# Kernel tuning notes

Measured on AMD Instinct MI355X. Metric: run time of the kernel, lower is better.

Reference implementation:

```python
import jax, jax.numpy as jnp
import numpy as np

EPS = 1e-06
N_HEADS = 8


def setup_inputs() -> dict:
    key = jax.random.key(0)
    ks = jax.random.split(key, 9)
    B, M, T, C = 2, 64, 256, 512
    s = 0.02
    return {
        "x": jax.random.normal(ks[0], (B, M, T, C), dtype=jnp.float32),
        "Wq": jax.random.normal(ks[1], (C, C), dtype=jnp.float32) * s,
        "bq": jnp.zeros((C,), dtype=jnp.float32),
        "Wk": jax.random.normal(ks[2], (C, C), dtype=jnp.float32) * s,
        "bk": jnp.zeros((C,), dtype=jnp.float32),
        "Wv": jax.random.normal(ks[3], (C, C), dtype=jnp.float32) * s,
        "bv": jnp.zeros((C,), dtype=jnp.float32),
        "Wp": jax.random.normal(ks[4], (C, C), dtype=jnp.float32) * s,
        "bp": jnp.zeros((C,), dtype=jnp.float32),
    }


def _proj_heads(x, W, b, N, D):
    # nn.Linear: x @ W.T + b, then view(B,M,T,N,D).transpose(2,3) -> [B,M,N,T,D]
    B, M, T, C = x.shape
    y = jnp.einsum('bmtc,dc->bmtd', x, W) + b
    return y.reshape(B, M, T, N, D).transpose(0, 1, 3, 2, 4)


def reference(x, Wq, bq, Wk, bk, Wv, bv, Wp, bp):
    B, M, T, C = x.shape
    N = N_HEADS
    D = C // N
    q = _proj_heads(x, Wq, bq, N, D)  # [B,M,N,T,D]
    k = _proj_heads(x, Wk, bk, N, D)
    v = _proj_heads(x, Wv, bv, N, D)
    # ELU+1 feature map
    q = jax.nn.elu(q) + 1.0
    k = jax.nn.elu(k) + 1.0
    # KtV = k^T @ v : [B,M,N,D,D]
    KtV = jnp.einsum('bmntd,bmnte->bmnde', k, v)
    # Z = 1 / (q @ sum_t k + eps) : [B,M,N,T]
    ksum = jnp.sum(k, axis=-2)  # [B,M,N,D]
    z = 1.0 / (jnp.einsum('bmntd,bmnd->bmnt', q, ksum) + EPS)
    # Original does Z.expand(...,D) @ KtV; since Z is constant over the D axis,
    # this equals z[t] * sum_d KtV[d, e] -- compute that directly (faithful math).
    KtV_colsum = jnp.sum(KtV, axis=-2)  # [B,M,N,D]
    V = z[..., None] * KtV_colsum[..., None, :]  # [B,M,N,T,D]
    V = V.transpose(0, 1, 3, 2, 4).reshape(B, M, T, N * D)
    out = jnp.einsum('bmtc,dc->bmtd', V, Wp) + bp
    return out
```

## Files before the change

### kernel.cpp

```cpp
#include <hip/hip_runtime.h>
#include <hip/hip_bf16.h>

#define BM_ 128
#define T_  256
#define C_  512
#define NH  8
#define DH  64

typedef __bf16 bf16;
typedef __attribute__((ext_vector_type(8))) __bf16 bf16x8;
typedef __attribute__((ext_vector_type(4))) float f32x4;

__device__ __forceinline__ float elu1(float v){ return v > 0.f ? v + 1.f : __expf(v); }

__device__ __forceinline__ unsigned short f2bf(float f){
  unsigned u = __float_as_uint(f);
  u += 0x7fffu + ((u >> 16) & 1u);
  return (unsigned short)(u >> 16);
}

__device__ __forceinline__ float bf2f(unsigned short b){
  return __uint_as_float(((unsigned)b) << 16);
}

#define GLOAD16(gptr, lptr) __builtin_amdgcn_global_load_lds( \
  (const __attribute__((address_space(1))) void*)(gptr), \
  (__attribute__((address_space(3))) void*)(lptr), 16, 0, 0)

#define FENCE() asm volatile("" ::: "memory")

__global__ __launch_bounds__(256) void cvt3_kernel(
    const float* __restrict__ a, int na4,
    const float* __restrict__ b, int nb4,
    const float* __restrict__ c, int nc4,
    unsigned short* __restrict__ oa, unsigned short* __restrict__ ob,
    unsigned short* __restrict__ oc)
{
  int i = blockIdx.x * blockDim.x + threadIdx.x;
  int stride = gridDim.x * blockDim.x;
  int total = na4 + nb4 + nc4;
  for (; i < total; i += stride) {
    const float* src; unsigned short* dst; int idx;
    if (i < na4)            { src = a; dst = oa; idx = i; }
    else if (i < na4 + nb4) { src = b; dst = ob; idx = i - na4; }
    else                    { src = c; dst = oc; idx = i - na4 - nb4; }
    float4 v = reinterpret_cast<const float4*>(src)[idx];
    ushort4 o;
    o.x = f2bf(v.x); o.y = f2bf(v.y); o.z = f2bf(v.z); o.w = f2bf(v.w);
    reinterpret_cast<ushort4*>(dst)[idx] = o;
  }
}

template<int MODE>
__global__ __launch_bounds__(512, 2) void gemm_proj(
    const bf16* __restrict__ A, const bf16* __restrict__ Bw,
    const float* __restrict__ bias,
    float* __restrict__ krow, float* __restrict__ ksum2,
    const float* __restrict__ ksum2_in, float* __restrict__ zden)
{
  __shared__ bf16 As[2][256 * 64];
  __shared__ bf16 Bs[2][256 * 64];

  const int tid  = threadIdx.x;
  const int lane = tid & 63;
  const int wid  = tid >> 6;
  const int wr   = wid >> 2, wc = wid & 3;

  const int L  = ((blockIdx.x & 7) << 5) + (blockIdx.x >> 3);
  const int tn = L & 1, tm = L >> 1;

  const bf16* Ab = A  + (size_t)(tm * 256) * C_;
  const bf16* Bb = Bw + (size_t)(tn * 256) * C_;

  const int srow  = tid >> 3;
  const int sslot = tid & 7;
  const int fr = lane & 15, fq = lane >> 4;

  f32x4 acc[8][4];
#pragma unroll
  for (int m = 0; m < 8; ++m)
#pragma unroll
    for (int n = 0; n < 4; ++n) acc[m][n] = (f32x4){0.f, 0.f, 0.f, 0.f};

#define STG(XS, Xb, b, h, kt) do { \
  _Pragma("unroll") \
  for (int q = 0; q < 2; ++q) { \
    int r_ = (h) * 128 + q * 64 + srow; \
    GLOAD16(Xb + (size_t)r_ * C_ + (kt) * 64 + ((sslot ^ (r_ & 7)) << 3), \
            &XS[b][(((h) * 128 + q * 64) << 6) + (tid << 3)]); \
  } } while (0)

#define LOFF(row, sl) (((row) << 6) + ((((sl) ^ ((row) & 7))) << 3))

  STG(As, Ab, 0, 0, 0); STG(As, Ab, 0, 1, 0);
  STG(Bs, Bb, 0, 0, 0); STG(Bs, Bb, 0, 1, 0);
  asm volatile("s_waitcnt vmcnt(0)" ::: "memory");
  __builtin_amdgcn_s_barrier();
  FENCE();

  bf16x8 af[4][2], bfr[4][2];

  for (int t = 0; t < 8; ++t) {
    const int cur = t & 1;
    const bool pre = (t < 7);
#pragma unroll
    for (int m = 0; m < 4; ++m)
#pragma unroll
      for (int kk = 0; kk < 2; ++kk) {
        int row = wr * 128 + m * 16 + fr;
        af[m][kk] = *reinterpret_cast<const bf16x8*>(&As[cur][LOFF(row, kk * 4 + fq)]);
      }
#pragma unroll
    for (int n = 0; n < 2; ++n)
#pragma unroll
      for (int kk = 0; kk < 2; ++kk) {
        int row = wc * 64 + n * 16 + fr;
        bfr[n][kk] = *reinterpret_cast<const bf16x8*>(&Bs[cur][LOFF(row, kk * 4 + fq)]);
      }
    if (pre) { STG(As, Ab, cur ^ 1, 0, t + 1); STG(Bs, Bb, cur ^ 1, 0, t + 1); }
    __builtin_amdgcn_s_setprio(1);
#pragma unroll
    for (int m = 0; m < 4; ++m)
#pragma unroll
      for (int n = 0; n < 2; ++n)
#pragma unroll
        for (int kk = 0; kk < 2; ++kk)
          acc[m][n] = __builtin_amdgcn_mfma_f32_16x16x32_bf16(af[m][kk], bfr[n][kk], acc[m][n], 0, 0, 0);
    __builtin_amdgcn_s_setprio(0);
    __builtin_amdgcn_s_barrier();
    FENCE();
#pragma unroll
    for (int n = 0; n < 2; ++n)
#pragma unroll
      for (int kk = 0; kk < 2; ++kk) {
        int row = wc * 64 + (n + 2) * 16 + fr;
        bfr[n + 2][kk] = *reinterpret_cast<const bf16x8*>(&Bs[cur][LOFF(row, kk * 4 + fq)]);
      }
    if (pre) STG(As, Ab, cur ^ 1, 1, t + 1);
    __builtin_amdgcn_s_setprio(1);
#pragma unroll
    for (int m = 0; m < 4; ++m)
#pragma unroll
      for (int n = 0; n < 2; ++n)
#pragma unroll
        for (int kk = 0; kk < 2; ++kk)
          acc[m][n + 2] = __builtin_amdgcn_mfma_f32_16x16x32_bf16(af[m][kk], bfr[n + 2][kk], acc[m][n + 2], 0, 0, 0);
    __builtin_amdgcn_s_setprio(0);
    __builtin_amdgcn_s_barrier();
    FENCE();
#pragma unroll
    for (int m = 0; m < 4; ++m)
#pragma unroll
      for (int kk = 0; kk < 2; ++kk) {
        int row = wr * 128 + 64 + m * 16 + fr;
        af[m][kk] = *reinterpret_cast<const bf16x8*>(&As[cur][LOFF(row, kk * 4 + fq)]);
      }
    if (pre) STG(Bs, Bb, cur ^ 1, 1, t + 1);
    __builtin_amdgcn_s_setprio(1);
#pragma unroll
    for (int m = 0; m < 4; ++m)
#pragma unroll
      for (int n = 0; n < 2; ++n)
#pragma unroll
        for (int kk = 0; kk < 2; ++kk)
          acc[m + 4][n] = __builtin_amdgcn_mfma_f32_16x16x32_bf16(af[m][kk], bfr[n][kk], acc[m + 4][n], 0, 0, 0);
    __builtin_amdgcn_s_setprio(0);
    __builtin_amdgcn_s_barrier();
    FENCE();
    __builtin_amdgcn_s_setprio(1);
#pragma unroll
    for (int m = 0; m < 4; ++m)
#pragma unroll
      for (int n = 0; n < 2; ++n)
#pragma unroll
        for (int kk = 0; kk < 2; ++kk)
          acc[m + 4][n + 2] = __builtin_amdgcn_mfma_f32_16x16x32_bf16(af[m][kk], bfr[n + 2][kk], acc[m + 4][n + 2], 0, 0, 0);
    __builtin_amdgcn_s_setprio(0);
    asm volatile("s_waitcnt vmcnt(0)" ::: "memory");
    __builtin_amdgcn_s_barrier();
    FENCE();
  }
#undef STG
#undef LOFF

  const int bm   = tm;
  const int head = tn * 4 + wc;
  float bj[4];
#pragma unroll
  for (int n = 0; n < 4; ++n) bj[n] = bias[tn * 256 + wc * 64 + n * 16 + fr];

  if (MODE == 0) {
    float cs[4] = {0.f, 0.f, 0.f, 0.f};
#pragma unroll
    for (int m = 0; m < 8; ++m) {
#pragma unroll
      for (int r = 0; r < 4; ++r) {
        float rs = 0.f;
#pragma unroll
        for (int n = 0; n < 4; ++n) {
          float v = elu1(acc[m][n][r] + bj[n]);
          rs += v;
          cs[n] += v;
        }
#pragma unroll
        for (int msk = 1; msk < 16; msk <<= 1) rs += __shfl_xor(rs, msk);
        if (fr == 0) {
          int tg = wr * 128 + m * 16 + fq * 4 + r;
          krow[((size_t)bm * NH + head) * T_ + tg] = rs;
        }
      }
    }
#pragma unroll
    for (int n = 0; n < 4; ++n) {
      cs[n] += __shfl_xor(cs[n], 16);
      cs[n] += __shfl_xor(cs[n], 32);
      if (fq == 0)
        ksum2[((size_t)wr * BM_ + bm) * C_ + tn * 256 + wc * 64 + n * 16 + fr] = cs[n];
    }
  } else {
    float ks[4];
#pragma unroll
    for (int n = 0; n < 4; ++n) {
      size_t col = (size_t)bm * C_ + tn * 256 + wc * 64 + n * 16 + fr;
      ks[n] = ksum2_in[col] + ksum2_in[(size_t)BM_ * C_ + col];
    }
#pragma unroll
    for (int m = 0; m < 8; ++m) {
#pragma unroll
      for (int r = 0; r < 4; ++r) {
        float zs = 0.f;
#pragma unroll
        for (int n = 0; n < 4; ++n) zs = fmaf(elu1(acc[m][n][r] + bj[n]), ks[n], zs);
#pragma unroll
        for (int msk = 1; msk < 16; msk <<= 1) zs += __shfl_xor(zs, msk);
        if (fr == 0) {
          int tg = wr * 128 + m * 16 + fq * 4 + r;
          zden[((size_t)bm * NH + head) * T_ + tg] = zs;
        }
      }
    }
  }
}

__global__ __launch_bounds__(256) void xk_kernel(
    const unsigned short* __restrict__ xb, const float* __restrict__ krow,
    float* __restrict__ xk4, float* __restrict__ srow4)
{
  const int bm = blockIdx.x, qt = blockIdx.y, tid = threadIdx.x;
  __shared__ float krs[NH * 64];
#pragma unroll
  for (int p = 0; p < 2; ++p) {
    int idx = tid + p * 256;
    int n = idx >> 6, t = idx & 63;
    krs[idx] = krow[((size_t)bm * NH + n) * T_ + qt * 64 + t];
  }
  __syncthreads();
  float a0[8], a1[8];
#pragma unroll
  for (int n = 0; n < 8; ++n) { a0[n] = 0.f; a1[n] = 0.f; }
  const unsigned short* xp = xb + ((size_t)bm * T_ + qt * 64) * C_ + tid * 2;
  for (int t = 0; t < 64; ++t) {
    ushort2 u = *reinterpret_cast<const ushort2*>(xp + (size_t)t * C_);
    float x0 = bf2f(u.x), x1 = bf2f(u.y);
#pragma unroll
    for (int n = 0; n < 8; ++n) {
      float kr = krs[n * 64 + t];
      a0[n] = fmaf(kr, x0, a0[n]);
      a1[n] = fmaf(kr, x1, a1[n]);
    }
  }
#pragma unroll
  for (int n = 0; n < 8; ++n)
    *reinterpret_cast<float2*>(&xk4[(((size_t)qt * BM_ + bm) * NH + n) * C_ + tid * 2])
        = make_float2(a0[n], a1[n]);
  if (tid < 8) {
    float s = 0.f;
    for (int t = 0; t < 64; ++t) s += krs[tid * 64 + t];
    srow4[((size_t)qt * BM_ + bm) * NH + tid] = s;
  }
}

__global__ __launch_bounds__(256) void colsum_kernel(
    const float* __restrict__ xk4, const float* __restrict__ srow4,
    const float* __restrict__ Wv, const float* __restrict__ bv,
    float* __restrict__ cs_g)
{
  const int bm0 = blockIdx.x * 8, h = blockIdx.y, tid = threadIdx.x;
  __shared__ float4 xs4[8][128];
#pragma unroll
  for (int p = 0; p < 4; ++p) {
    int idx = tid + p * 256;
    int bmr = idx >> 7, c4 = idx & 127;
    float4 s = make_float4(0.f, 0.f, 0.f, 0.f);
#pragma unroll
    for (int q = 0; q < 4; ++q) {
      float4 u = *reinterpret_cast<const float4*>(
          xk4 + (((size_t)q * BM_ + bm0 + bmr) * NH + h) * C_ + c4 * 4);
      s.x += u.x; s.y += u.y; s.z += u.z; s.w += u.w;
    }
    xs4[bmr][c4] = s;
  }
  __syncthreads();
  const int e = tid & 63, bs = tid >> 6;
  const float4* wv4 = reinterpret_cast<const float4*>(Wv + (size_t)(h * DH + e) * C_);
  float acc0 = 0.f, acc1 = 0.f;
#pragma unroll 4
  for (int c4 = 0; c4 < 128; ++c4) {
    float4 w = wv4[c4];
    float4 a = xs4[bs * 2][c4];
    float4 b = xs4[bs * 2 + 1][c4];
    acc0 += w.x * a.x + w.y * a.y + w.z * a.z + w.w * a.w;
    acc1 += w.x * b.x + w.y * b.y + w.z * b.z + w.w * b.w;
  }
  float bve = bv[h * DH + e];
  int bmA = bm0 + bs * 2, bmB = bmA + 1;
  float sA = 0.f, sB = 0.f;
#pragma unroll
  for (int q = 0; q < 4; ++q) {
    sA += srow4[((size_t)q * BM_ + bmA) * NH + h];
    sB += srow4[((size_t)q * BM_ + bmB) * NH + h];
  }
  cs_g[((size_t)bmA * NH + h) * DH + e] = acc0 + sA * bve;
  cs_g[((size_t)bmB * NH + h) * DH + e] = acc1 + sB * bve;
}

__global__ __launch_bounds__(256) void wbuf_kernel(
    const float* __restrict__ cs_g, const float* __restrict__ Wp,
    float* __restrict__ wbuf)
{
  const int cpt = blockIdx.x, h = blockIdx.y, bm0 = blockIdx.z * 16;
  const int tid = threadIdx.x;
  __shared__ float4 csL4[16][16];
  {
    int bmr = tid >> 4, e4 = tid & 15;
    csL4[bmr][e4] = *reinterpret_cast<const float4*>(
        cs_g + ((size_t)(bm0 + bmr) * NH + h) * DH + e4 * 4);
  }
  __syncthreads();
  const int cp = cpt * 256 + tid;
  float4 wp[16];
  const float4* wpr = reinterpret_cast<const float4*>(Wp + (size_t)cp * C_ + h * DH);
#pragma unroll
  for (int e4 = 0; e4 < 16; ++e4) wp[e4] = wpr[e4];
#pragma unroll
  for (int bmr = 0; bmr < 16; ++bmr) {
    float acc = 0.f;
#pragma unroll
    for (int e4 = 0; e4 < 16; ++e4) {
      float4 c = csL4[bmr][e4];
      acc += wp[e4].x * c.x + wp[e4].y * c.y + wp[e4].z * c.z + wp[e4].w * c.w;
    }
    wbuf[((size_t)(bm0 + bmr) * NH + h) * C_ + cp] = acc;
  }
}

__global__ __launch_bounds__(256) void out_kernel(
    const float* __restrict__ zden, const float* __restrict__ wbuf,
    const float* __restrict__ bp, float* __restrict__ out)
{
  const int bm = blockIdx.x, tt = blockIdx.y, tid = threadIdx.x;
  __shared__ float zs[NH][64];
#pragma unroll
  for (int p = 0; p < 2; ++p) {
    int idx = tid + p * 256;
    int n = idx >> 6, t = idx & 63;
    zs[n][t] = 1.f / (zden[((size_t)bm * NH + n) * T_ + tt * 64 + t] + 1e-6f);
  }
  float2 wv[8];
  const int c2 = tid * 2;
#pragma unroll
  for (int n = 0; n < 8; ++n)
    wv[n] = *reinterpret_cast<const float2*>(wbuf + ((size_t)bm * NH + n) * C_ + c2);
  float2 bpv = *reinterpret_cast<const float2*>(bp + c2);
  __syncthreads();
  float* ob = out + ((size_t)bm * T_ + tt * 64) * C_;
  for (int t = 0; t < 64; ++t) {
    float o0 = bpv.x, o1 = bpv.y;
#pragma unroll
    for (int n = 0; n < 8; ++n) { float z = zs[n][t]; o0 = fmaf(z, wv[n].x, o0); o1 = fmaf(z, wv[n].y, o1); }
    *reinterpret_cast<float2*>(ob + (size_t)t * C_ + c2) = make_float2(o0, o1);
  }
}

extern "C" void kernel_launch(void* const* d_in, const int* in_sizes, int n_in,
                              void* d_out, int out_size, void* d_ws, size_t ws_size,
                              hipStream_t stream)
{
  const float* x  = (const float*)d_in[0];
  const float* Wq = (const float*)d_in[1];
  const float* bq = (const float*)d_in[2];
  const float* Wk = (const float*)d_in[3];
  const float* bk = (const float*)d_in[4];
  const float* Wv = (const float*)d_in[5];
  const float* bv = (const float*)d_in[6];
  const float* Wp = (const float*)d_in[7];
  const float* bp = (const float*)d_in[8];
  float* out = (float*)d_out;

  float* ws    = (float*)d_ws;
  float* zden  = ws;
  float* ksum2 = zden + 262144;
  float* krow  = ksum2 + 131072;
  float* srow4 = krow + 262144;
  float* xk4   = srow4 + 4096;
  float* cs    = xk4 + 2097152;
  float* wbuf  = cs + 65536;
  unsigned short* xb  = (unsigned short*)(wbuf + 524288);
  unsigned short* wkb = xb + 16777216;
  unsigned short* wqb = wkb + 262144;

  cvt3_kernel<<<2048, 256, 0, stream>>>(x, 16777216 / 4, Wk, 262144 / 4, Wq, 262144 / 4,
                                        xb, wkb, wqb);

  gemm_proj<0><<<256, 512, 0, stream>>>((const bf16*)xb, (const bf16*)wkb, bk,
                                        krow, ksum2, nullptr, nullptr);
  xk_kernel<<<dim3(BM_, 4), 256, 0, stream>>>(xb, krow, xk4, srow4);
  colsum_kernel<<<dim3(16, 8), 256, 0, stream>>>(xk4, srow4, Wv, bv, cs);
  wbuf_kernel<<<dim3(2, 8, 8), 256, 0, stream>>>(cs, Wp, wbuf);
  gemm_proj<1><<<256, 512, 0, stream>>>((const bf16*)xb, (const bf16*)wqb, bq,
                                        nullptr, nullptr, ksum2, zden);
  out_kernel<<<dim3(BM_, 4), 256, 0, stream>>>(zden, wbuf, bp, out);
}
```

Before: 115.9 us.

## Fuse x fp32-to-bf16 conversion into K projection GEMM and merge colsum/wbuf kernels

The first projection GEMM now reads fp32 x directly through registers, converts it to bf16, writes it into LDS, and also stores the bf16 copy to global memory (only from tn==0 blocks) for later kernels. This removes the separate full pass that converted x, and that pass's extra launch. The V-projection colsum and the Wp weighting kernels are merged into one kernel that keeps the intermediate column sums in shared memory. The trade-offs are more register pressure and a loss of asynchronous LDS loads for A in the MODE 0 GEMM, and the merged kernel launches only 64 blocks, which reduces parallelism.

```diff
diff --git a/kernel.cpp b/kernel.cpp
--- a/kernel.cpp
+++ b/kernel.cpp
@@ -29,32 +29,25 @@
 
 #define FENCE() asm volatile("" ::: "memory")
 
-__global__ __launch_bounds__(256) void cvt3_kernel(
-    const float* __restrict__ a, int na4,
-    const float* __restrict__ b, int nb4,
-    const float* __restrict__ c, int nc4,
-    unsigned short* __restrict__ oa, unsigned short* __restrict__ ob,
-    unsigned short* __restrict__ oc)
-{
-  int i = blockIdx.x * blockDim.x + threadIdx.x;
-  int stride = gridDim.x * blockDim.x;
-  int total = na4 + nb4 + nc4;
-  for (; i < total; i += stride) {
-    const float* src; unsigned short* dst; int idx;
-    if (i < na4)            { src = a; dst = oa; idx = i; }
-    else if (i < na4 + nb4) { src = b; dst = ob; idx = i - na4; }
-    else                    { src = c; dst = oc; idx = i - na4 - nb4; }
-    float4 v = reinterpret_cast<const float4*>(src)[idx];
-    ushort4 o;
-    o.x = f2bf(v.x); o.y = f2bf(v.y); o.z = f2bf(v.z); o.w = f2bf(v.w);
-    reinterpret_cast<ushort4*>(dst)[idx] = o;
-  }
+__global__ __launch_bounds__(256) void wcvt_kernel(
+    const float* __restrict__ wk, const float* __restrict__ wq,
+    unsigned short* __restrict__ ok, unsigned short* __restrict__ oq)
+{
+  int i = blockIdx.x * 256 + threadIdx.x;
+  float4 v = reinterpret_cast<const float4*>(wk)[i];
+  ushort4 o;
+  o.x = f2bf(v.x); o.y = f2bf(v.y); o.z = f2bf(v.z); o.w = f2bf(v.w);
+  reinterpret_cast<ushort4*>(ok)[i] = o;
+  v = reinterpret_cast<const float4*>(wq)[i];
+  o.x = f2bf(v.x); o.y = f2bf(v.y); o.z = f2bf(v.z); o.w = f2bf(v.w);
+  reinterpret_cast<ushort4*>(oq)[i] = o;
 }
 
 template<int MODE>
 __global__ __launch_bounds__(512, 2) void gemm_proj(
-    const bf16* __restrict__ A, const bf16* __restrict__ Bw,
-    const float* __restrict__ bias,
+    const bf16* __restrict__ A, const float* __restrict__ Axf,
+    unsigned short* __restrict__ xbout,
+    const bf16* __restrict__ Bw, const float* __restrict__ bias,
     float* __restrict__ krow, float* __restrict__ ksum2,
     const float* __restrict__ ksum2_in, float* __restrict__ zden)
 {
@@ -92,9 +85,40 @@
 
 #define LOFF(row, sl) (((row) << 6) + ((((sl) ^ ((row) & 7))) << 3))
 
-  STG(As, Ab, 0, 0, 0); STG(As, Ab, 0, 1, 0);
-  STG(Bs, Bb, 0, 0, 0); STG(Bs, Bb, 0, 1, 0);
-  asm volatile("s_waitcnt vmcnt(0)" ::: "memory");
+#define AISSUE(LO, HI, h, kt) do { \
+  _Pragma("unroll") \
+  for (int q = 0; q < 2; ++q) { \
+    int r_ = (h) * 128 + q * 64 + srow; \
+    const float* gp = Axf + (size_t)(tm * 256 + r_) * C_ + (kt) * 64 + sslot * 8; \
+    LO[q] = *reinterpret_cast<const float4*>(gp); \
+    HI[q] = *reinterpret_cast<const float4*>(gp + 4); \
+  } } while (0)
+
+#define AWRITE(LO, HI, b, h, kt) do { \
+  _Pragma("unroll") \
+  for (int q = 0; q < 2; ++q) { \
+    int r_ = (h) * 128 + q * 64 + srow; \
+    uint4 v; \
+    v.x = (unsigned)f2bf(LO[q].x) | ((unsigned)f2bf(LO[q].y) << 16); \
+    v.y = (unsigned)f2bf(LO[q].z) | ((unsigned)f2bf(LO[q].w) << 16); \
+    v.z = (unsigned)f2bf(HI[q].x) | ((unsigned)f2bf(HI[q].y) << 16); \
+    v.w = (unsigned)f2bf(HI[q].z) | ((unsigned)f2bf(HI[q].w) << 16); \
+    *reinterpret_cast<uint4*>(&As[b][LOFF(r_, sslot)]) = v; \
+    if (tn == 0) \
+      *reinterpret_cast<uint4*>(xbout + (size_t)(tm * 256 + r_) * C_ + (kt) * 64 + sslot * 8) = v; \
+  } } while (0)
+
+  float4 a0l[2], a0h[2], a1l[2], a1h[2];
+
+  if constexpr (MODE == 0) {
+    AISSUE(a0l, a0h, 0, 0); AISSUE(a1l, a1h, 1, 0);
+    STG(Bs, Bb, 0, 0, 0);   STG(Bs, Bb, 0, 1, 0);
+    AWRITE(a0l, a0h, 0, 0, 0); AWRITE(a1l, a1h, 0, 1, 0);
+  } else {
+    STG(As, Ab, 0, 0, 0); STG(As, Ab, 0, 1, 0);
+    STG(Bs, Bb, 0, 0, 0); STG(Bs, Bb, 0, 1, 0);
+  }
+  asm volatile("s_waitcnt vmcnt(0) lgkmcnt(0)" ::: "memory");
   __builtin_amdgcn_s_barrier();
   FENCE();
 
@@ -117,7 +141,11 @@
         int row = wc * 64 + n * 16 + fr;
         bfr[n][kk] = *reinterpret_cast<const bf16x8*>(&Bs[cur][LOFF(row, kk * 4 + fq)]);
       }
-    if (pre) { STG(As, Ab, cur ^ 1, 0, t + 1); STG(Bs, Bb, cur ^ 1, 0, t + 1); }
+    if (pre) {
+      if constexpr (MODE == 0) AISSUE(a0l, a0h, 0, t + 1);
+      else                     STG(As, Ab, cur ^ 1, 0, t + 1);
+      STG(Bs, Bb, cur ^ 1, 0, t + 1);
+    }
     __builtin_amdgcn_s_setprio(1);
 #pragma unroll
     for (int m = 0; m < 4; ++m)
@@ -136,7 +164,11 @@
         int row = wc * 64 + (n + 2) * 16 + fr;
         bfr[n + 2][kk] = *reinterpret_cast<const bf16x8*>(&Bs[cur][LOFF(row, kk * 4 + fq)]);
       }
-    if (pre) STG(As, Ab, cur ^ 1, 1, t + 1);
+    if (pre) {
+      if constexpr (MODE == 0) AISSUE(a1l, a1h, 1, t + 1);
+      else                     STG(As, Ab, cur ^ 1, 1, t + 1);
+      STG(Bs, Bb, cur ^ 1, 1, t + 1);
+    }
     __builtin_amdgcn_s_setprio(1);
 #pragma unroll
     for (int m = 0; m < 4; ++m)
@@ -155,7 +187,7 @@
         int row = wr * 128 + 64 + m * 16 + fr;
         af[m][kk] = *reinterpret_cast<const bf16x8*>(&As[cur][LOFF(row, kk * 4 + fq)]);
       }
-    if (pre) STG(Bs, Bb, cur ^ 1, 1, t + 1);
+    if (pre) { if constexpr (MODE == 0) AWRITE(a0l, a0h, cur ^ 1, 0, t + 1); }
     __builtin_amdgcn_s_setprio(1);
 #pragma unroll
     for (int m = 0; m < 4; ++m)
@@ -167,6 +199,7 @@
     __builtin_amdgcn_s_setprio(0);
     __builtin_amdgcn_s_barrier();
     FENCE();
+    if (pre) { if constexpr (MODE == 0) AWRITE(a1l, a1h, cur ^ 1, 1, t + 1); }
     __builtin_amdgcn_s_setprio(1);
 #pragma unroll
     for (int m = 0; m < 4; ++m)
@@ -176,12 +209,14 @@
         for (int kk = 0; kk < 2; ++kk)
           acc[m + 4][n + 2] = __builtin_amdgcn_mfma_f32_16x16x32_bf16(af[m][kk], bfr[n + 2][kk], acc[m + 4][n + 2], 0, 0, 0);
     __builtin_amdgcn_s_setprio(0);
-    asm volatile("s_waitcnt vmcnt(0)" ::: "memory");
+    asm volatile("s_waitcnt vmcnt(0) lgkmcnt(0)" ::: "memory");
     __builtin_amdgcn_s_barrier();
     FENCE();
   }
 #undef STG
 #undef LOFF
+#undef AISSUE
+#undef AWRITE
 
   const int bm   = tm;
   const int head = tn * 4 + wc;
@@ -280,15 +315,16 @@
   }
 }
 
-__global__ __launch_bounds__(256) void colsum_kernel(
+__global__ __launch_bounds__(256) void vproj_kernel(
     const float* __restrict__ xk4, const float* __restrict__ srow4,
     const float* __restrict__ Wv, const float* __restrict__ bv,
-    float* __restrict__ cs_g)
-{
-  const int bm0 = blockIdx.x * 8, h = blockIdx.y, tid = threadIdx.x;
-  __shared__ float4 xs4[8][128];
-#pragma unroll
-  for (int p = 0; p < 4; ++p) {
+    const float* __restrict__ Wp, float* __restrict__ wbuf)
+{
+  const int bm0 = blockIdx.x * 16, h = blockIdx.y, tid = threadIdx.x;
+  __shared__ float4 xs4[16][128];
+  __shared__ float cs[16][DH];
+#pragma unroll
+  for (int p = 0; p < 8; ++p) {
     int idx = tid + p * 256;
     int bmr = idx >> 7, c4 = idx & 127;
     float4 s = make_float4(0.f, 0.f, 0.f, 0.f);
@@ -301,56 +337,47 @@
     xs4[bmr][c4] = s;
   }
   __syncthreads();
-  const int e = tid & 63, bs = tid >> 6;
-  const float4* wv4 = reinterpret_cast<const float4*>(Wv + (size_t)(h * DH + e) * C_);
-  float acc0 = 0.f, acc1 = 0.f;
+  {
+    const int e = tid & 63, g = tid >> 6;
+    const float4* wv4 = reinterpret_cast<const float4*>(Wv + (size_t)(h * DH + e) * C_);
+    float acc[4] = {0.f, 0.f, 0.f, 0.f};
 #pragma unroll 4
-  for (int c4 = 0; c4 < 128; ++c4) {
-    float4 w = wv4[c4];
-    float4 a = xs4[bs * 2][c4];
-    float4 b = xs4[bs * 2 + 1][c4];
-    acc0 += w.x * a.x + w.y * a.y + w.z * a.z + w.w * a.w;
-    acc1 += w.x * b.x + w.y * b.y + w.z * b.z + w.w * b.w;
-  }
-  float bve = bv[h * DH + e];
-  int bmA = bm0 + bs * 2, bmB = bmA + 1;
-  float sA = 0.f, sB = 0.f;
-#pragma unroll
-  for (int q = 0; q < 4; ++q) {
-    sA += srow4[((size_t)q * BM_ + bmA) * NH + h];
-    sB += srow4[((size_t)q * BM_ + bmB) * NH + h];
-  }
-  cs_g[((size_t)bmA * NH + h) * DH + e] = acc0 + sA * bve;
-  cs_g[((size_t)bmB * NH + h) * DH + e] = acc1 + sB * bve;
-}
-
-__global__ __launch_bounds__(256) void wbuf_kernel(
-    const float* __restrict__ cs_g, const float* __restrict__ Wp,
-    float* __restrict__ wbuf)
-{
-  const int cpt = blockIdx.x, h = blockIdx.y, bm0 = blockIdx.z * 16;
-  const int tid = threadIdx.x;
-  __shared__ float4 csL4[16][16];
-  {
-    int bmr = tid >> 4, e4 = tid & 15;
-    csL4[bmr][e4] = *reinterpret_cast<const float4*>(
-        cs_g + ((size_t)(bm0 + bmr) * NH + h) * DH + e4 * 4);
+    for (int c4 = 0; c4 < 128; ++c4) {
+      float4 w = wv4[c4];
+#pragma unroll
+      for (int i = 0; i < 4; ++i) {
+        float4 a = xs4[g * 4 + i][c4];
+        acc[i] += w.x * a.x + w.y * a.y + w.z * a.z + w.w * a.w;
+      }
+    }
+    float bve = bv[h * DH + e];
+#pragma unroll
+    for (int i = 0; i < 4; ++i) {
+      int bm = bm0 + g * 4 + i;
+      float s = 0.f;
+#pragma unroll
+      for (int q = 0; q < 4; ++q) s += srow4[((size_t)q * BM_ + bm) * NH + h];
+      cs[g * 4 + i][e] = acc[i] + s * bve;
+    }
   }
   __syncthreads();
-  const int cp = cpt * 256 + tid;
-  float4 wp[16];
-  const float4* wpr = reinterpret_cast<const float4*>(Wp + (size_t)cp * C_ + h * DH);
-#pragma unroll
-  for (int e4 = 0; e4 < 16; ++e4) wp[e4] = wpr[e4];
-#pragma unroll
-  for (int bmr = 0; bmr < 16; ++bmr) {
-    float acc = 0.f;
-#pragma unroll
-    for (int e4 = 0; e4 < 16; ++e4) {
-      float4 c = csL4[bmr][e4];
-      acc += wp[e4].x * c.x + wp[e4].y * c.y + wp[e4].z * c.z + wp[e4].w * c.w;
-    }
-    wbuf[((size_t)(bm0 + bmr) * NH + h) * C_ + cp] = acc;
+#pragma unroll
+  for (int cph = 0; cph < 2; ++cph) {
+    int cp = cph * 256 + tid;
+    const float4* wpr = reinterpret_cast<const float4*>(Wp + (size_t)cp * C_ + h * DH);
+    float4 wp[16];
+#pragma unroll
+    for (int e4 = 0; e4 < 16; ++e4) wp[e4] = wpr[e4];
+#pragma unroll
+    for (int bmr = 0; bmr < 16; ++bmr) {
+      const float* ch = cs[bmr];
+      float acc = 0.f;
+#pragma unroll
+      for (int e4 = 0; e4 < 16; ++e4)
+        acc += wp[e4].x * ch[e4 * 4] + wp[e4].y * ch[e4 * 4 + 1]
+             + wp[e4].z * ch[e4 * 4 + 2] + wp[e4].w * ch[e4 * 4 + 3];
+      wbuf[((size_t)(bm0 + bmr) * NH + h) * C_ + cp] = acc;
+    }
   }
 }
 
@@ -403,21 +430,19 @@
   float* krow  = ksum2 + 131072;
   float* srow4 = krow + 262144;
   float* xk4   = srow4 + 4096;
-  float* cs    = xk4 + 2097152;
-  float* wbuf  = cs + 65536;
+  float* wbuf  = xk4 + 2097152;
   unsigned short* xb  = (unsigned short*)(wbuf + 524288);
   unsigned short* wkb = xb + 16777216;
   unsigned short* wqb = wkb + 262144;
 
-  cvt3_kernel<<<2048, 256, 0, stream>>>(x, 16777216 / 4, Wk, 262144 / 4, Wq, 262144 / 4,
-                                        xb, wkb, wqb);
-
-  gemm_proj<0><<<256, 512, 0, stream>>>((const bf16*)xb, (const bf16*)wkb, bk,
+  wcvt_kernel<<<256, 256, 0, stream>>>(Wk, Wq, wkb, wqb);
+
+  gemm_proj<0><<<256, 512, 0, stream>>>(nullptr, x, xb, (const bf16*)wkb, bk,
                                         krow, ksum2, nullptr, nullptr);
   xk_kernel<<<dim3(BM_, 4), 256, 0, stream>>>(xb, krow, xk4, srow4);
-  colsum_kernel<<<dim3(16, 8), 256, 0, stream>>>(xk4, srow4, Wv, bv, cs);
-  wbuf_kernel<<<dim3(2, 8, 8), 256, 0, stream>>>(cs, Wp, wbuf);
-  gemm_proj<1><<<256, 512, 0, stream>>>((const bf16*)xb, (const bf16*)wqb, bq,
-                                        nullptr, nullptr, ksum2, zden);
+  vproj_kernel<<<dim3(8, 8), 256, 0, stream>>>(xk4, srow4, Wv, bv, Wp, wbuf);
+  gemm_proj<1><<<256, 512, 0, stream>>>((const bf16*)xb, nullptr, nullptr,
+                                        (const bf16*)wqb, bq,
+                                        nullptr, ksum2, ksum2, zden);
   out_kernel<<<dim3(BM_, 4), 256, 0, stream>>>(zden, wbuf, bp, out);
 }
```

After: 260.6 us. 125% more time.

## Shrink projection GEMM tiles to 256x128 with K=32 steps for higher occupancy

Applied to the files above, without the earlier changes.

Reworks the bf16 MFMA projection GEMM from 256x256 tiles with K-step 64 to 256x128 tiles with K-step 32. This halves LDS use and accumulators, raises launch bounds to 4 blocks per CU, and doubles the grid to 512 blocks. The key column partial sums are now split into four row-slices instead of two, and the Q pass sums all four. It aims for better CU fill and latency hiding, at the cost of lower per-block data reuse, more global traffic and twice as many barriers per K loop.

```diff
diff --git a/kernel.cpp b/kernel.cpp
--- a/kernel.cpp
+++ b/kernel.cpp
@@ -52,147 +52,94 @@
 }
 
 template<int MODE>
-__global__ __launch_bounds__(512, 2) void gemm_proj(
+__global__ __launch_bounds__(512, 4) void gemm_proj(
     const bf16* __restrict__ A, const bf16* __restrict__ Bw,
     const float* __restrict__ bias,
-    float* __restrict__ krow, float* __restrict__ ksum2,
-    const float* __restrict__ ksum2_in, float* __restrict__ zden)
-{
-  __shared__ bf16 As[2][256 * 64];
-  __shared__ bf16 Bs[2][256 * 64];
+    float* __restrict__ krow, float* __restrict__ ksum4,
+    const float* __restrict__ ksum4_in, float* __restrict__ zden)
+{
+  __shared__ bf16 As[2][256 * 32];
+  __shared__ bf16 Bs[2][128 * 32];
 
   const int tid  = threadIdx.x;
   const int lane = tid & 63;
   const int wid  = tid >> 6;
-  const int wr   = wid >> 2, wc = wid & 3;
-
-  const int L  = ((blockIdx.x & 7) << 5) + (blockIdx.x >> 3);
-  const int tn = L & 1, tm = L >> 1;
+  const int wr   = wid >> 1, wc = wid & 1;
+
+  const int L  = ((blockIdx.x & 7) << 6) + (blockIdx.x >> 3);
+  const int tn = L & 3, tm = L >> 2;
 
   const bf16* Ab = A  + (size_t)(tm * 256) * C_;
-  const bf16* Bb = Bw + (size_t)(tn * 256) * C_;
-
-  const int srow  = tid >> 3;
-  const int sslot = tid & 7;
+  const bf16* Bb = Bw + (size_t)(tn * 128) * C_;
   const int fr = lane & 15, fq = lane >> 4;
 
-  f32x4 acc[8][4];
-#pragma unroll
-  for (int m = 0; m < 8; ++m)
+  f32x4 acc[4][4];
+#pragma unroll
+  for (int m = 0; m < 4; ++m)
 #pragma unroll
     for (int n = 0; n < 4; ++n) acc[m][n] = (f32x4){0.f, 0.f, 0.f, 0.f};
 
-#define STG(XS, Xb, b, h, kt) do { \
+#define SW(r, s) ((s) ^ (((r) ^ ((r) >> 2)) & 3))
+#define LOFF(row, sl) ((row) * 32 + (SW(row, sl) << 3))
+
+#define STGA(b, kt) do { \
   _Pragma("unroll") \
-  for (int q = 0; q < 2; ++q) { \
-    int r_ = (h) * 128 + q * 64 + srow; \
-    GLOAD16(Xb + (size_t)r_ * C_ + (kt) * 64 + ((sslot ^ (r_ & 7)) << 3), \
-            &XS[b][(((h) * 128 + q * 64) << 6) + (tid << 3)]); \
+  for (int j = 0; j < 2; ++j) { \
+    int d_ = j * 512 + tid; int r_ = d_ >> 2; int s_ = d_ & 3; \
+    GLOAD16(Ab + (size_t)r_ * C_ + (kt) * 32 + (SW(r_, s_) << 3), \
+            &As[b][d_ * 8]); \
   } } while (0)
 
-#define LOFF(row, sl) (((row) << 6) + ((((sl) ^ ((row) & 7))) << 3))
-
-  STG(As, Ab, 0, 0, 0); STG(As, Ab, 0, 1, 0);
-  STG(Bs, Bb, 0, 0, 0); STG(Bs, Bb, 0, 1, 0);
+#define STGB(b, kt) do { \
+    int r_ = tid >> 2; int s_ = tid & 3; \
+    GLOAD16(Bb + (size_t)r_ * C_ + (kt) * 32 + (SW(r_, s_) << 3), \
+            &Bs[b][tid * 8]); \
+  } while (0)
+
+  STGA(0, 0); STGB(0, 0);
   asm volatile("s_waitcnt vmcnt(0)" ::: "memory");
   __builtin_amdgcn_s_barrier();
   FENCE();
 
-  bf16x8 af[4][2], bfr[4][2];
-
-  for (int t = 0; t < 8; ++t) {
+  bf16x8 af[4], bfr[4];
+
+  for (int t = 0; t < 16; ++t) {
     const int cur = t & 1;
-    const bool pre = (t < 7);
 #pragma unroll
     for (int m = 0; m < 4; ++m)
-#pragma unroll
-      for (int kk = 0; kk < 2; ++kk) {
-        int row = wr * 128 + m * 16 + fr;
-        af[m][kk] = *reinterpret_cast<const bf16x8*>(&As[cur][LOFF(row, kk * 4 + fq)]);
-      }
-#pragma unroll
-    for (int n = 0; n < 2; ++n)
-#pragma unroll
-      for (int kk = 0; kk < 2; ++kk) {
-        int row = wc * 64 + n * 16 + fr;
-        bfr[n][kk] = *reinterpret_cast<const bf16x8*>(&Bs[cur][LOFF(row, kk * 4 + fq)]);
-      }
-    if (pre) { STG(As, Ab, cur ^ 1, 0, t + 1); STG(Bs, Bb, cur ^ 1, 0, t + 1); }
+      af[m] = *reinterpret_cast<const bf16x8*>(&As[cur][LOFF(wr * 64 + m * 16 + fr, fq)]);
+#pragma unroll
+    for (int n = 0; n < 4; ++n)
+      bfr[n] = *reinterpret_cast<const bf16x8*>(&Bs[cur][LOFF(wc * 64 + n * 16 + fr, fq)]);
+    if (t < 15) { STGA(cur ^ 1, t + 1); STGB(cur ^ 1, t + 1); }
     __builtin_amdgcn_s_setprio(1);
 #pragma unroll
     for (int m = 0; m < 4; ++m)
 #pragma unroll
-      for (int n = 0; n < 2; ++n)
-#pragma unroll
-        for (int kk = 0; kk < 2; ++kk)
-          acc[m][n] = __builtin_amdgcn_mfma_f32_16x16x32_bf16(af[m][kk], bfr[n][kk], acc[m][n], 0, 0, 0);
+      for (int n = 0; n < 4; ++n)
+        acc[m][n] = __builtin_amdgcn_mfma_f32_16x16x32_bf16(af[m], bfr[n], acc[m][n], 0, 0, 0);
     __builtin_amdgcn_s_setprio(0);
-    __builtin_amdgcn_s_barrier();
-    FENCE();
-#pragma unroll
-    for (int n = 0; n < 2; ++n)
-#pragma unroll
-      for (int kk = 0; kk < 2; ++kk) {
-        int row = wc * 64 + (n + 2) * 16 + fr;
-        bfr[n + 2][kk] = *reinterpret_cast<const bf16x8*>(&Bs[cur][LOFF(row, kk * 4 + fq)]);
-      }
-    if (pre) STG(As, Ab, cur ^ 1, 1, t + 1);
-    __builtin_amdgcn_s_setprio(1);
-#pragma unroll
-    for (int m = 0; m < 4; ++m)
-#pragma unroll
-      for (int n = 0; n < 2; ++n)
-#pragma unroll
-        for (int kk = 0; kk < 2; ++kk)
-          acc[m][n + 2] = __builtin_amdgcn_mfma_f32_16x16x32_bf16(af[m][kk], bfr[n + 2][kk], acc[m][n + 2], 0, 0, 0);
-    __builtin_amdgcn_s_setprio(0);
-    __builtin_amdgcn_s_barrier();
-    FENCE();
-#pragma unroll
-    for (int m = 0; m < 4; ++m)
-#pragma unroll
-      for (int kk = 0; kk < 2; ++kk) {
-        int row = wr * 128 + 64 + m * 16 + fr;
-        af[m][kk] = *reinterpret_cast<const bf16x8*>(&As[cur][LOFF(row, kk * 4 + fq)]);
-      }
-    if (pre) STG(Bs, Bb, cur ^ 1, 1, t + 1);
-    __builtin_amdgcn_s_setprio(1);
-#pragma unroll
-    for (int m = 0; m < 4; ++m)
-#pragma unroll
-      for (int n = 0; n < 2; ++n)
-#pragma unroll
-        for (int kk = 0; kk < 2; ++kk)
-          acc[m + 4][n] = __builtin_amdgcn_mfma_f32_16x16x32_bf16(af[m][kk], bfr[n][kk], acc[m + 4][n], 0, 0, 0);
-    __builtin_amdgcn_s_setprio(0);
-    __builtin_amdgcn_s_barrier();
-    FENCE();
-    __builtin_amdgcn_s_setprio(1);
-#pragma unroll
-    for (int m = 0; m < 4; ++m)
-#pragma unroll
-      for (int n = 0; n < 2; ++n)
-#pragma unroll
-        for (int kk = 0; kk < 2; ++kk)
-          acc[m + 4][n + 2] = __builtin_amdgcn_mfma_f32_16x16x32_bf16(af[m][kk], bfr[n + 2][kk], acc[m + 4][n + 2], 0, 0, 0);
-    __builtin_amdgcn_s_setprio(0);
-    asm volatile("s_waitcnt vmcnt(0)" ::: "memory");
-    __builtin_amdgcn_s_barrier();
-    FENCE();
-  }
-#undef STG
+    if (t < 15) {
+      asm volatile("s_waitcnt vmcnt(0)" ::: "memory");
+      __builtin_amdgcn_s_barrier();
+      FENCE();
+    }
+  }
+#undef STGA
+#undef STGB
 #undef LOFF
+#undef SW
 
   const int bm   = tm;
-  const int head = tn * 4 + wc;
+  const int head = tn * 2 + wc;
   float bj[4];
 #pragma unroll
-  for (int n = 0; n < 4; ++n) bj[n] = bias[tn * 256 + wc * 64 + n * 16 + fr];
+  for (int n = 0; n < 4; ++n) bj[n] = bias[tn * 128 + wc * 64 + n * 16 + fr];
 
   if (MODE == 0) {
     float cs[4] = {0.f, 0.f, 0.f, 0.f};
 #pragma unroll
-    for (int m = 0; m < 8; ++m) {
+    for (int m = 0; m < 4; ++m) {
 #pragma unroll
       for (int r = 0; r < 4; ++r) {
         float rs = 0.f;
@@ -205,7 +152,7 @@
 #pragma unroll
         for (int msk = 1; msk < 16; msk <<= 1) rs += __shfl_xor(rs, msk);
         if (fr == 0) {
-          int tg = wr * 128 + m * 16 + fq * 4 + r;
+          int tg = wr * 64 + m * 16 + fq * 4 + r;
           krow[((size_t)bm * NH + head) * T_ + tg] = rs;
         }
       }
@@ -215,17 +162,18 @@
       cs[n] += __shfl_xor(cs[n], 16);
       cs[n] += __shfl_xor(cs[n], 32);
       if (fq == 0)
-        ksum2[((size_t)wr * BM_ + bm) * C_ + tn * 256 + wc * 64 + n * 16 + fr] = cs[n];
+        ksum4[((size_t)wr * BM_ + bm) * C_ + tn * 128 + wc * 64 + n * 16 + fr] = cs[n];
     }
   } else {
     float ks[4];
 #pragma unroll
     for (int n = 0; n < 4; ++n) {
-      size_t col = (size_t)bm * C_ + tn * 256 + wc * 64 + n * 16 + fr;
-      ks[n] = ksum2_in[col] + ksum2_in[(size_t)BM_ * C_ + col];
-    }
-#pragma unroll
-    for (int m = 0; m < 8; ++m) {
+      size_t col = (size_t)bm * C_ + tn * 128 + wc * 64 + n * 16 + fr;
+      ks[n] = ksum4_in[col] + ksum4_in[(size_t)BM_ * C_ + col]
+            + ksum4_in[2 * (size_t)BM_ * C_ + col] + ksum4_in[3 * (size_t)BM_ * C_ + col];
+    }
+#pragma unroll
+    for (int m = 0; m < 4; ++m) {
 #pragma unroll
       for (int r = 0; r < 4; ++r) {
         float zs = 0.f;
@@ -234,7 +182,7 @@
 #pragma unroll
         for (int msk = 1; msk < 16; msk <<= 1) zs += __shfl_xor(zs, msk);
         if (fr == 0) {
-          int tg = wr * 128 + m * 16 + fq * 4 + r;
+          int tg = wr * 64 + m * 16 + fq * 4 + r;
           zden[((size_t)bm * NH + head) * T_ + tg] = zs;
         }
       }
@@ -399,8 +347,8 @@
 
   float* ws    = (float*)d_ws;
   float* zden  = ws;
-  float* ksum2 = zden + 262144;
-  float* krow  = ksum2 + 131072;
+  float* ksum4 = zden + 262144;
+  float* krow  = ksum4 + 262144;
   float* srow4 = krow + 262144;
   float* xk4   = srow4 + 4096;
   float* cs    = xk4 + 2097152;
@@ -412,12 +360,12 @@
   cvt3_kernel<<<2048, 256, 0, stream>>>(x, 16777216 / 4, Wk, 262144 / 4, Wq, 262144 / 4,
                                         xb, wkb, wqb);
 
-  gemm_proj<0><<<256, 512, 0, stream>>>((const bf16*)xb, (const bf16*)wkb, bk,
-                                        krow, ksum2, nullptr, nullptr);
+  gemm_proj<0><<<512, 512, 0, stream>>>((const bf16*)xb, (const bf16*)wkb, bk,
+                                        krow, ksum4, nullptr, nullptr);
   xk_kernel<<<dim3(BM_, 4), 256, 0, stream>>>(xb, krow, xk4, srow4);
   colsum_kernel<<<dim3(16, 8), 256, 0, stream>>>(xk4, srow4, Wv, bv, cs);
   wbuf_kernel<<<dim3(2, 8, 8), 256, 0, stream>>>(cs, Wp, wbuf);
-  gemm_proj<1><<<256, 512, 0, stream>>>((const bf16*)xb, (const bf16*)wqb, bq,
-                                        nullptr, nullptr, ksum2, zden);
+  gemm_proj<1><<<512, 512, 0, stream>>>((const bf16*)xb, (const bf16*)wqb, bq,
+                                        nullptr, ksum4, ksum4, zden);
   out_kernel<<<dim3(BM_, 4), 256, 0, stream>>>(zden, wbuf, bp, out);
 }
```

Measured after the change: 116.6 us. Within noise of the previous version (+0.6%).

## Split GEMM k-tile into half-slices and prefetch two stages ahead

Applied to the files above, without the earlier changes.

Reworks the shared-memory layout of the projection GEMM so each 64-wide k-tile is stored as two 32-wide halves, each with its own XOR swizzle. Loads for the next tile are issued one half at a time, up to two half-stages ahead, and the loop waits with vmcnt(4) instead of fully draining each iteration. Barriers per iteration drop from four to two and fragment registers shrink. The aim is to hide global-load latency behind MFMA work, at the cost of more complex vmcnt bookkeeping and a different bank-conflict pattern. The MODE 1 launch now also passes ksum2 in the ksum2 slot instead of nullptr.

```diff
diff --git a/kernel.cpp b/kernel.cpp
--- a/kernel.cpp
+++ b/kernel.cpp
@@ -58,8 +58,8 @@
     float* __restrict__ krow, float* __restrict__ ksum2,
     const float* __restrict__ ksum2_in, float* __restrict__ zden)
 {
-  __shared__ bf16 As[2][256 * 64];
-  __shared__ bf16 Bs[2][256 * 64];
+  __shared__ bf16 As[2][2 * 8192];
+  __shared__ bf16 Bs[2][2 * 8192];
 
   const int tid  = threadIdx.x;
   const int lane = tid & 63;
@@ -71,9 +71,6 @@
 
   const bf16* Ab = A  + (size_t)(tm * 256) * C_;
   const bf16* Bb = Bw + (size_t)(tn * 256) * C_;
-
-  const int srow  = tid >> 3;
-  const int sslot = tid & 7;
   const int fr = lane & 15, fq = lane >> 4;
 
   f32x4 acc[8][4];
@@ -82,101 +79,83 @@
 #pragma unroll
     for (int n = 0; n < 4; ++n) acc[m][n] = (f32x4){0.f, 0.f, 0.f, 0.f};
 
-#define STG(XS, Xb, b, h, kt) do { \
+#define LOFF(kk, row, sl) ((kk) * 8192 + (row) * 32 + ((((sl) ^ (((row) >> 1) & 3))) << 3))
+
+#define STG(XS, Xb, b, kk, kt) do { \
   _Pragma("unroll") \
-  for (int q = 0; q < 2; ++q) { \
-    int r_ = (h) * 128 + q * 64 + srow; \
-    GLOAD16(Xb + (size_t)r_ * C_ + (kt) * 64 + ((sslot ^ (r_ & 7)) << 3), \
-            &XS[b][(((h) * 128 + q * 64) << 6) + (tid << 3)]); \
+  for (int j = 0; j < 2; ++j) { \
+    int d_ = j * 512 + tid; int r_ = d_ >> 2; int s_ = d_ & 3; \
+    GLOAD16(Xb + (size_t)r_ * C_ + (kt) * 64 + (kk) * 32 + (((s_ ^ ((r_ >> 1) & 3))) << 3), \
+            &XS[b][(kk) * 8192 + d_ * 8]); \
   } } while (0)
 
-#define LOFF(row, sl) (((row) << 6) + ((((sl) ^ ((row) & 7))) << 3))
-
-  STG(As, Ab, 0, 0, 0); STG(As, Ab, 0, 1, 0);
-  STG(Bs, Bb, 0, 0, 0); STG(Bs, Bb, 0, 1, 0);
-  asm volatile("s_waitcnt vmcnt(0)" ::: "memory");
+  STG(As, Ab, 0, 0, 0); STG(Bs, Bb, 0, 0, 0);
+  STG(As, Ab, 0, 1, 0); STG(Bs, Bb, 0, 1, 0);
+  STG(As, Ab, 1, 0, 1); STG(Bs, Bb, 1, 0, 1);
+  asm volatile("s_waitcnt vmcnt(4)" ::: "memory");
   __builtin_amdgcn_s_barrier();
   FENCE();
 
-  bf16x8 af[4][2], bfr[4][2];
+  bf16x8 af[4], bfr[4];
 
   for (int t = 0; t < 8; ++t) {
     const int cur = t & 1;
-    const bool pre = (t < 7);
-#pragma unroll
-    for (int m = 0; m < 4; ++m)
-#pragma unroll
-      for (int kk = 0; kk < 2; ++kk) {
-        int row = wr * 128 + m * 16 + fr;
-        af[m][kk] = *reinterpret_cast<const bf16x8*>(&As[cur][LOFF(row, kk * 4 + fq)]);
-      }
-#pragma unroll
-    for (int n = 0; n < 2; ++n)
-#pragma unroll
-      for (int kk = 0; kk < 2; ++kk) {
-        int row = wc * 64 + n * 16 + fr;
-        bfr[n][kk] = *reinterpret_cast<const bf16x8*>(&Bs[cur][LOFF(row, kk * 4 + fq)]);
-      }
-    if (pre) { STG(As, Ab, cur ^ 1, 0, t + 1); STG(Bs, Bb, cur ^ 1, 0, t + 1); }
+
+#pragma unroll
+    for (int m = 0; m < 4; ++m)
+      af[m] = *reinterpret_cast<const bf16x8*>(&As[cur][LOFF(0, wr * 128 + m * 16 + fr, fq)]);
+#pragma unroll
+    for (int n = 0; n < 4; ++n)
+      bfr[n] = *reinterpret_cast<const bf16x8*>(&Bs[cur][LOFF(0, wc * 64 + n * 16 + fr, fq)]);
+    if (t + 1 < 8) { STG(As, Ab, cur ^ 1, 1, t + 1); STG(Bs, Bb, cur ^ 1, 1, t + 1); }
     __builtin_amdgcn_s_setprio(1);
 #pragma unroll
     for (int m = 0; m < 4; ++m)
 #pragma unroll
-      for (int n = 0; n < 2; ++n)
-#pragma unroll
-        for (int kk = 0; kk < 2; ++kk)
-          acc[m][n] = __builtin_amdgcn_mfma_f32_16x16x32_bf16(af[m][kk], bfr[n][kk], acc[m][n], 0, 0, 0);
+      for (int n = 0; n < 4; ++n)
+        acc[m][n] = __builtin_amdgcn_mfma_f32_16x16x32_bf16(af[m], bfr[n], acc[m][n], 0, 0, 0);
+    __builtin_amdgcn_s_setprio(0);
+
+#pragma unroll
+    for (int m = 0; m < 4; ++m)
+      af[m] = *reinterpret_cast<const bf16x8*>(&As[cur][LOFF(0, wr * 128 + 64 + m * 16 + fr, fq)]);
+    __builtin_amdgcn_s_setprio(1);
+#pragma unroll
+    for (int m = 0; m < 4; ++m)
+#pragma unroll
+      for (int n = 0; n < 4; ++n)
+        acc[m + 4][n] = __builtin_amdgcn_mfma_f32_16x16x32_bf16(af[m], bfr[n], acc[m + 4][n], 0, 0, 0);
     __builtin_amdgcn_s_setprio(0);
     __builtin_amdgcn_s_barrier();
     FENCE();
-#pragma unroll
-    for (int n = 0; n < 2; ++n)
-#pragma unroll
-      for (int kk = 0; kk < 2; ++kk) {
-        int row = wc * 64 + (n + 2) * 16 + fr;
-        bfr[n + 2][kk] = *reinterpret_cast<const bf16x8*>(&Bs[cur][LOFF(row, kk * 4 + fq)]);
-      }
-    if (pre) STG(As, Ab, cur ^ 1, 1, t + 1);
+
+#pragma unroll
+    for (int m = 0; m < 4; ++m)
+      af[m] = *reinterpret_cast<const bf16x8*>(&As[cur][LOFF(1, wr * 128 + m * 16 + fr, fq)]);
+#pragma unroll
+    for (int n = 0; n < 4; ++n)
+      bfr[n] = *reinterpret_cast<const bf16x8*>(&Bs[cur][LOFF(1, wc * 64 + n * 16 + fr, fq)]);
+    if (t + 2 < 8) { STG(As, Ab, cur, 0, t + 2); STG(Bs, Bb, cur, 0, t + 2); }
     __builtin_amdgcn_s_setprio(1);
 #pragma unroll
     for (int m = 0; m < 4; ++m)
 #pragma unroll
-      for (int n = 0; n < 2; ++n)
-#pragma unroll
-        for (int kk = 0; kk < 2; ++kk)
-          acc[m][n + 2] = __builtin_amdgcn_mfma_f32_16x16x32_bf16(af[m][kk], bfr[n + 2][kk], acc[m][n + 2], 0, 0, 0);
+      for (int n = 0; n < 4; ++n)
+        acc[m][n] = __builtin_amdgcn_mfma_f32_16x16x32_bf16(af[m], bfr[n], acc[m][n], 0, 0, 0);
     __builtin_amdgcn_s_setprio(0);
-    __builtin_amdgcn_s_barrier();
-    FENCE();
-#pragma unroll
-    for (int m = 0; m < 4; ++m)
-#pragma unroll
-      for (int kk = 0; kk < 2; ++kk) {
-        int row = wr * 128 + 64 + m * 16 + fr;
-        af[m][kk] = *reinterpret_cast<const bf16x8*>(&As[cur][LOFF(row, kk * 4 + fq)]);
-      }
-    if (pre) STG(Bs, Bb, cur ^ 1, 1, t + 1);
+
+#pragma unroll
+    for (int m = 0; m < 4; ++m)
+      af[m] = *reinterpret_cast<const bf16x8*>(&As[cur][LOFF(1, wr * 128 + 64 + m * 16 + fr, fq)]);
     __builtin_amdgcn_s_setprio(1);
 #pragma unroll
     for (int m = 0; m < 4; ++m)
 #pragma unroll
-      for (int n = 0; n < 2; ++n)
-#pragma unroll
-        for (int kk = 0; kk < 2; ++kk)
-          acc[m + 4][n] = __builtin_amdgcn_mfma_f32_16x16x32_bf16(af[m][kk], bfr[n][kk], acc[m + 4][n], 0, 0, 0);
+      for (int n = 0; n < 4; ++n)
+        acc[m + 4][n] = __builtin_amdgcn_mfma_f32_16x16x32_bf16(af[m], bfr[n], acc[m + 4][n], 0, 0, 0);
     __builtin_amdgcn_s_setprio(0);
-    __builtin_amdgcn_s_barrier();
-    FENCE();
-    __builtin_amdgcn_s_setprio(1);
-#pragma unroll
-    for (int m = 0; m < 4; ++m)
-#pragma unroll
-      for (int n = 0; n < 2; ++n)
-#pragma unroll
-        for (int kk = 0; kk < 2; ++kk)
-          acc[m + 4][n + 2] = __builtin_amdgcn_mfma_f32_16x16x32_bf16(af[m][kk], bfr[n + 2][kk], acc[m + 4][n + 2], 0, 0, 0);
-    __builtin_amdgcn_s_setprio(0);
-    asm volatile("s_waitcnt vmcnt(0)" ::: "memory");
+    if (t < 6)      asm volatile("s_waitcnt vmcnt(4)" ::: "memory");
+    else if (t == 6) asm volatile("s_waitcnt vmcnt(0)" ::: "memory");
     __builtin_amdgcn_s_barrier();
     FENCE();
   }
@@ -418,6 +397,6 @@
   colsum_kernel<<<dim3(16, 8), 256, 0, stream>>>(xk4, srow4, Wv, bv, cs);
   wbuf_kernel<<<dim3(2, 8, 8), 256, 0, stream>>>(cs, Wp, wbuf);
   gemm_proj<1><<<256, 512, 0, stream>>>((const bf16*)xb, (const bf16*)wqb, bq,
-                                        nullptr, nullptr, ksum2, zden);
+                                        nullptr, ksum2, ksum2, zden);
   out_kernel<<<dim3(BM_, 4), 256, 0, stream>>>(zden, wbuf, bp, out);
 }
```

New measurement: 118.8 us. 1.02x slower.
